# Performance work log

Hardware: AMD Instinct MI355X
Metric: run time of the kernel (lower is better)

## Reference

```python
import jax, jax.numpy as jnp
import numpy as np

B, SQ, SK, D, H = 2, 2048, 2048, 1024, 16
DK = D // H


def setup_inputs() -> dict:
    key = jax.random.key(0)
    ks = jax.random.split(key, 16)
    s = 1.0 / np.sqrt(D)
    inp = {
        "query": jax.random.normal(ks[0], (B, SQ, D), jnp.float32),
        "key": jax.random.normal(ks[1], (B, SK, D), jnp.float32),
        "value": jax.random.normal(ks[2], (B, SK, D), jnp.float32),
        "R": jax.random.normal(ks[3], (B, SK, D), jnp.float32),
        "Wq": jax.random.normal(ks[4], (D, D), jnp.float32) * s,
        "bq": jnp.zeros((D,), jnp.float32),
        "Wv": jax.random.normal(ks[5], (D, D), jnp.float32) * s,
        "bv": jnp.zeros((D,), jnp.float32),
        "Wr": jax.random.normal(ks[6], (D, D), jnp.float32) * s,
        "br": jnp.zeros((D,), jnp.float32),
        "W_h": jax.random.normal(ks[7], (H, DK, DK), jnp.float32) * (1.0 / np.sqrt(DK)),
        "Wo": jax.random.normal(ks[8], (D, D), jnp.float32) * s,
        "bo": jnp.zeros((D,), jnp.float32),
    }
    return inp


def _forward(query, key, value, R, Wq, bq, Wv, bv, Wr, br, W_h, Wo, bo):
    scale = 1.0 / np.sqrt(DK)
    # projections (torch Linear: x @ W.T + b)
    Q = (query @ Wq.T + bq).reshape(B, SQ, H, DK).transpose(0, 2, 1, 3)   # (B,H,SQ,DK)
    V = (value @ Wv.T + bv).reshape(B, SK, H, DK).transpose(0, 2, 1, 3)   # (B,H,SK,DK)
    Rp = (R @ Wr.T + br).reshape(B, SK, H, DK).transpose(0, 2, 1, 3)      # (B,H,SK,DK)
    # torch einsum 'hnk,bhn->bhn' sums W_h over its last axis -> elementwise gate
    w_rowsum = W_h.sum(axis=-1)  # (H, DK)

    def step(h, r_t):
        h_new = jnp.tanh(h * w_rowsum + r_t)  # (B,H,DK)
        return h_new, h_new

    h0 = jnp.zeros((B, H, DK), Rp.dtype)
    Rt = Rp.transpose(2, 0, 1, 3)  # (SK,B,H,DK)
    _, Hs = jax.lax.scan(step, h0, Rt)
    Hst = Hs.transpose(1, 2, 0, 3)  # (B,H,SK,DK)

    scores = jnp.einsum('bhqd,bhkd->bhqk', Q, Hst) * scale
    attn = jax.nn.softmax(scores, axis=-1)
    out = jnp.einsum('bhqk,bhkd->bhqd', attn, V)
    out = out.transpose(0, 2, 1, 3).reshape(B, SQ, D)
    return out @ Wo.T + bo


def reference(query, key, value, R, Wq, bq, Wv, bv, Wr, br, W_h, Wo, bo):
    return _forward(query, key, value, R, Wq, bq, Wv, bv, Wr, br, W_h, Wo, bo)
```

## Files before the change

### kernel.cpp

```cpp
#include <hip/hip_runtime.h>
#include <stdint.h>

typedef unsigned short u16;
typedef __attribute__((ext_vector_type(8))) _Float16 h8;
typedef __attribute__((ext_vector_type(2))) __fp16 hp2;
typedef __attribute__((ext_vector_type(4))) float f4;

#define B_ 2
#define SQ_ 2048
#define SK_ 2048
#define D_ 1024
#define H_ 16
#define DK_ 64

__device__ __forceinline__ u16 f2h(float f) {
  union { _Float16 h; u16 u; } v; v.h = (_Float16)f; return v.u;
}
__device__ __forceinline__ float h2f(u16 b) {
  union { u16 u; _Float16 h; } v; v.u = b; return (float)v.h;
}
__device__ __forceinline__ unsigned pkrtz(float a, float b) {
  union { hp2 h; unsigned u; } v; v.h = __builtin_amdgcn_cvt_pkrtz(a, b); return v.u;
}
__device__ __forceinline__ float fexp2(float x) {
  float r;
  asm("v_exp_f32 %0, %1" : "=v"(r) : "v"(x));
  return r;
}

typedef const void __attribute__((address_space(1)))* gas1;
typedef void __attribute__((address_space(3)))* las3;
__device__ __forceinline__ void gld16(const void* g, void* l) {
  __builtin_amdgcn_global_load_lds((gas1)g, (las3)l, 16, 0, 0);
}

__device__ __forceinline__ void cast8(const float* __restrict__ src,
                                      u16* __restrict__ dst, int i) {
  float4 a = *(const float4*)(src + i);
  float4 b = *(const float4*)(src + i + 4);
  alignas(16) u16 t[8] = {f2h(a.x), f2h(a.y), f2h(a.z), f2h(a.w),
                          f2h(b.x), f2h(b.y), f2h(b.z), f2h(b.w)};
  *(int4*)(dst + i) = *(int4*)t;
}

__global__ void rma_cast_rwr(const float* __restrict__ xr, const float* __restrict__ wr,
                             u16* __restrict__ orr, u16* __restrict__ owr) {
  const int b = blockIdx.x;
  const float* src; u16* dst; int bi;
  if (b < 2048) { src = xr; dst = orr; bi = b; }
  else          { src = wr; dst = owr; bi = b - 2048; }
  cast8(src, dst, (bi * 256 + threadIdx.x) * 8);
}

__device__ __forceinline__ void gemm_mainloop(
    const u16* __restrict__ A, const u16* __restrict__ Bw, int K,
    u16* As, u16* Bs, int m0, int n0, f4 (&acc)[4][4]) {
  const int tid = threadIdx.x;
  const int w = tid >> 6, lane = tid & 63;
  const int quad = lane >> 4, ln = lane & 15;
  const int wm = (w >> 1) * 64, wn = (w & 1) * 64;
  const int c0 = tid, c1 = tid + 256;
  const u16* a0 = A + (size_t)(m0 + (c0 >> 2)) * K + (c0 & 3) * 8;
  const u16* a1 = A + (size_t)(m0 + (c1 >> 2)) * K + (c1 & 3) * 8;
  const u16* b0 = Bw + (size_t)(n0 + (c0 >> 2)) * K + (c0 & 3) * 8;
  const u16* b1 = Bw + (size_t)(n0 + (c1 >> 2)) * K + (c1 & 3) * 8;
  u16* As0 = As + (0 + w * 64) * 8;
  u16* As1 = As + (256 + w * 64) * 8;
  u16* Bs0 = Bs + (0 + w * 64) * 8;
  u16* Bs1 = Bs + (256 + w * 64) * 8;
  for (int kt = 0; kt < K; kt += 32) {
    gld16(a0 + kt, As0);
    gld16(a1 + kt, As1);
    gld16(b0 + kt, Bs0);
    gld16(b1 + kt, Bs1);
    __syncthreads();
    h8 af[4], bf[4];
#pragma unroll
    for (int i = 0; i < 4; i++)
      af[i] = *(const h8*)&As[(wm + i * 16 + ln) * 32 + quad * 8];
#pragma unroll
    for (int i = 0; i < 4; i++)
      bf[i] = *(const h8*)&Bs[(wn + i * 16 + ln) * 32 + quad * 8];
#pragma unroll
    for (int i = 0; i < 4; i++)
#pragma unroll
      for (int j = 0; j < 4; j++)
        acc[i][j] = __builtin_amdgcn_mfma_f32_16x16x32_f16(af[i], bf[j], acc[i][j], 0, 0, 0);
    __syncthreads();
  }
}

__device__ __forceinline__ void gemm_mainloop64(
    const u16* __restrict__ A, const u16* __restrict__ Bw, int K,
    u16* As, u16* Bs, int m0, int n0, f4 (&acc)[2][4]) {
  const int tid = threadIdx.x;
  const int w = tid >> 6, lane = tid & 63;
  const int quad = lane >> 4, ln = lane & 15;
  const int wm = (w >> 1) * 32, wn = (w & 1) * 64;
  const u16* a0 = A + (size_t)(m0 + (tid >> 2)) * K + (tid & 3) * 8;
  const u16* b0 = Bw + (size_t)(n0 + (tid >> 2)) * K + (tid & 3) * 8;
  const u16* b1 = Bw + (size_t)(n0 + ((tid + 256) >> 2)) * K + (tid & 3) * 8;
  u16* As0 = As + (w * 64) * 8;
  u16* Bs0 = Bs + (w * 64) * 8;
  u16* Bs1 = Bs + (256 + w * 64) * 8;
  for (int kt = 0; kt < K; kt += 32) {
    gld16(a0 + kt, As0);
    gld16(b0 + kt, Bs0);
    gld16(b1 + kt, Bs1);
    __syncthreads();
    h8 af[2], bf[4];
#pragma unroll
    for (int i = 0; i < 2; i++)
      af[i] = *(const h8*)&As[(wm + i * 16 + ln) * 32 + quad * 8];
#pragma unroll
    for (int j = 0; j < 4; j++)
      bf[j] = *(const h8*)&Bs[(wn + j * 16 + ln) * 32 + quad * 8];
#pragma unroll
    for (int i = 0; i < 2; i++)
#pragma unroll
      for (int j = 0; j < 4; j++)
        acc[i][j] = __builtin_amdgcn_mfma_f32_16x16x32_f16(af[i], bf[j], acc[i][j], 0, 0, 0);
    __syncthreads();
  }
}

__global__ __launch_bounds__(256, 2)
void rma_projr_cast(const u16* __restrict__ Xr, const u16* __restrict__ Wrb,
                    const float* __restrict__ br, float* __restrict__ Rp,
                    const float* __restrict__ xq, const float* __restrict__ xv,
                    const float* __restrict__ wq, const float* __restrict__ wv,
                    const float* __restrict__ wo, u16* __restrict__ oxq,
                    u16* __restrict__ oxv, u16* __restrict__ owq,
                    u16* __restrict__ owv, u16* __restrict__ owo) {
  __shared__ u16 As[128 * 32];
  __shared__ u16 Bs[128 * 32];
  const int b = blockIdx.x;
  if (b >= 256) {
    const int c = b - 256;
    const float* src; u16* dst; int bi;
    if (c < 2048)       { src = xq; dst = oxq; bi = c; }
    else if (c < 4096)  { src = xv; dst = oxv; bi = c - 2048; }
    else if (c < 4608)  { src = wq; dst = owq; bi = c - 4096; }
    else if (c < 5120)  { src = wv; dst = owv; bi = c - 4608; }
    else                { src = wo; dst = owo; bi = c - 5120; }
    cast8(src, dst, (bi * 256 + threadIdx.x) * 8);
    return;
  }
  const int m0 = (b & 31) * 128, n0 = (b >> 5) * 128;
  f4 acc[4][4] = {};
  gemm_mainloop(Xr, Wrb, D_, As, Bs, m0, n0, acc);
  const int tid = threadIdx.x;
  const int w = tid >> 6, lane = tid & 63;
  const int quad = lane >> 4, ln = lane & 15;
  const int wm = (w >> 1) * 64, wn = (w & 1) * 64;
#pragma unroll
  for (int i = 0; i < 4; i++)
#pragma unroll
    for (int j = 0; j < 4; j++) {
      const int colg = n0 + wn + j * 16 + ln;
      const float bb = br[colg];
      const int h = colg >> 6, d = colg & 63;
      const int row4 = m0 + wm + i * 16 + quad * 4;
      const int bb_i = row4 >> 11, s = row4 & 2047;
#pragma unroll
      for (int r = 0; r < 4; r++) {
        const size_t idx = ((size_t)(bb_i * H_ + h) * SK_ + (s + r)) * DK_ + d;
        Rp[idx] = acc[i][j][r] + bb;
      }
    }
}

#define RB_ 32
__global__ __launch_bounds__(256, 1)
void rma_recur_projqv(const float* __restrict__ Rp, const float* __restrict__ Wh,
                      u16* __restrict__ Hst, const u16* __restrict__ Xq,
                      const u16* __restrict__ Xv, const u16* __restrict__ Wqb,
                      const u16* __restrict__ Wvb, const float* __restrict__ bq,
                      const float* __restrict__ bv, u16* __restrict__ Qb,
                      u16* __restrict__ Vt) {
  __shared__ u16 As[128 * 32];
  __shared__ u16 Bs[128 * 32];
  const int blk = blockIdx.x;
  if (blk < 8) {
    __builtin_amdgcn_s_setprio(2);
    const int ch = blk * 256 + threadIdx.x;
    const int bh = ch >> 6, d = ch & 63, h = bh & 15;
    const float* wr = Wh + (h * 64 + d) * 64;
    float ws = 0.f;
#pragma unroll
    for (int k = 0; k < 64; k += 4) {
      float4 wv4 = *(const float4*)(wr + k);
      ws += (wv4.x + wv4.y) + (wv4.z + wv4.w);
    }
    const float C2 = 2.885390081777927f;
    const float wsC2 = ws * C2;
    const float Kw = 2.0f * wsC2;
    const size_t base = (size_t)bh * (SK_ * DK_) + d;
    const float* r = Rp + base;
    u16* o = Hst + base;
    float cur[RB_], nxt[RB_];
#pragma unroll
    for (int j = 0; j < RB_; j++) cur[j] = r[(size_t)j * DK_];
    float e = fexp2(cur[0] * C2);
    for (int t0 = 0; t0 < SK_; t0 += RB_) {
      const int tn = (t0 + RB_ < SK_) ? (t0 + RB_) : t0;
#pragma unroll
      for (int j = 0; j < RB_; j++) nxt[j] = r[(size_t)(tn + j) * DK_];
#pragma unroll
      for (int j = 0; j < RB_; j++) {
        const float a = e + 1.0f;
        const float bb = __builtin_amdgcn_rcpf(a);
        const float hs = __builtin_fmaf(-2.0f, bb, 1.0f);
        o[(size_t)(t0 + j) * DK_] = f2h(hs);
        const float rn = (j + 1 < RB_) ? cur[j + 1] : nxt[0];
        const float K = __builtin_fmaf(C2, rn, wsC2);
        const float x = __builtin_fmaf(-Kw, bb, K);
        e = fexp2(x);
      }
#pragma unroll
      for (int j = 0; j < RB_; j++) cur[j] = nxt[j];
    }
    return;
  }
  const int pb = blk - 8;
  const int z = pb >> 8;
  const int t = pb & 255;
  const int m0 = (t & 31) * 128, n0 = (t >> 5) * 128;
  const u16* A = z == 0 ? Xq : Xv;
  const u16* Bw = z == 0 ? Wqb : Wvb;
  const float* bias = z == 0 ? bq : bv;
  f4 acc[4][4] = {};
  gemm_mainloop(A, Bw, D_, As, Bs, m0, n0, acc);
  const int tid = threadIdx.x;
  const int w = tid >> 6, lane = tid & 63;
  const int quad = lane >> 4, ln = lane & 15;
  const int wm = (w >> 1) * 64, wn = (w & 1) * 64;
#pragma unroll
  for (int i = 0; i < 4; i++)
#pragma unroll
    for (int j = 0; j < 4; j++) {
      const int colg = n0 + wn + j * 16 + ln;
      const float bb = bias[colg];
      const int h = colg >> 6, d = colg & 63;
      const int row4 = m0 + wm + i * 16 + quad * 4;
      const int b = row4 >> 11, s = row4 & 2047;
      if (z == 1) {
        uint2 pk;
        pk.x = pkrtz(acc[i][j][0] + bb, acc[i][j][1] + bb);
        pk.y = pkrtz(acc[i][j][2] + bb, acc[i][j][3] + bb);
        *(uint2*)&Vt[((size_t)((b * H_ + h) * DK_ + d)) * SK_ + s] = pk;
      } else {
#pragma unroll
        for (int r = 0; r < 4; r++) {
          const float v = acc[i][j][r] + bb;
          const size_t idx = ((size_t)(b * H_ + h) * SK_ + (s + r)) * DK_ + d;
          Qb[idx] = f2h(v);
        }
      }
    }
}

__global__ __launch_bounds__(256, 2)
void rma_final_gemm(const u16* __restrict__ Og, const u16* __restrict__ Wo,
                    const float* __restrict__ bo, float* __restrict__ out) {
  __shared__ u16 As[64 * 32];
  __shared__ u16 Bs[128 * 32];
  const int m0 = blockIdx.x * 64, n0 = blockIdx.y * 128;
  f4 acc[2][4] = {};
  gemm_mainloop64(Og, Wo, D_, As, Bs, m0, n0, acc);
  const int tid = threadIdx.x;
  const int w = tid >> 6, lane = tid & 63;
  const int quad = lane >> 4, ln = lane & 15;
  const int wm = (w >> 1) * 32, wn = (w & 1) * 64;
#pragma unroll
  for (int i = 0; i < 2; i++)
#pragma unroll
    for (int j = 0; j < 4; j++) {
      const int colg = n0 + wn + j * 16 + ln;
      const float bb = bo[colg];
#pragma unroll
      for (int r = 0; r < 4; r++) {
        const int rowg = m0 + wm + i * 16 + quad * 4 + r;
        out[(size_t)rowg * D_ + colg] = acc[i][j][r] + bb;
      }
    }
}

#define FXM_ 12.0f
__global__ __launch_bounds__(256, 2)
void rma_flash(const u16* __restrict__ Qb, const u16* __restrict__ Hst,
               const u16* __restrict__ Vt, u16* __restrict__ Og) {
  __shared__ u16 Kt[64 * 72];
  __shared__ u16 Vts[64 * 72];
  __shared__ u16 Ps[4][32 * 72];
  const int tid = threadIdx.x;
  const int w = tid >> 6, lane = tid & 63;
  const int quad = lane >> 4, ln = lane & 15;
  const int bh = blockIdx.y;
  const int q0 = blockIdx.x * 128 + w * 32;
  const float scale2 = 0.18033688011112042f;
  const u16* Qg = Qb + (size_t)bh * SQ_ * DK_;
  const u16* Kg = Hst + (size_t)bh * SK_ * DK_;
  const u16* Vg = Vt + (size_t)bh * DK_ * SK_;
  u16* Pw = Ps[w];
  h8 qf[2][2];
#pragma unroll
  for (int qt = 0; qt < 2; qt++)
#pragma unroll
    for (int c = 0; c < 2; c++)
      qf[qt][c] = *(const h8*)&Qg[(size_t)(q0 + qt * 16 + ln) * DK_ + c * 32 + quad * 8];
  f4 o[4][2] = {};
  float l[2] = {0.f, 0.f};

  const int c0 = tid, c1 = tid + 256;
  const int r0 = c0 >> 3, o0 = (c0 & 7) * 8;
  const int r1 = c1 >> 3, o1 = (c1 & 7) * 8;
  const u16* kg0 = Kg + (size_t)r0 * DK_ + o0;
  const u16* kg1 = Kg + (size_t)r1 * DK_ + o1;
  const u16* vg0 = Vg + (size_t)r0 * SK_ + o0;
  const u16* vg1 = Vg + (size_t)r1 * SK_ + o1;
  u16* kl0 = &Kt[r0 * 72 + o0];
  u16* kl1 = &Kt[r1 * 72 + o1];
  u16* vl0 = &Vts[r0 * 72 + o0];
  u16* vl1 = &Vts[r1 * 72 + o1];

  int4 ks0 = *(const int4*)(kg0);
  int4 ks1 = *(const int4*)(kg1);
  int4 vs0 = *(const int4*)(vg0);
  int4 vs1 = *(const int4*)(vg1);

  for (int kt = 0; kt < SK_; kt += 64) {
    __syncthreads();
    *(int4*)kl0 = ks0;
    *(int4*)kl1 = ks1;
    *(int4*)vl0 = vs0;
    *(int4*)vl1 = vs1;
    __syncthreads();
    h8 kf[4][2], vf[4][2];
#pragma unroll
    for (int m = 0; m < 4; m++) {
      kf[m][0] = *(const h8*)&Kt[(m * 16 + ln) * 72 + quad * 8];
      kf[m][1] = *(const h8*)&Kt[(m * 16 + ln) * 72 + 32 + quad * 8];
    }
#pragma unroll
    for (int dt = 0; dt < 4; dt++) {
      vf[dt][0] = *(const h8*)&Vts[(dt * 16 + ln) * 72 + quad * 8];
      vf[dt][1] = *(const h8*)&Vts[(dt * 16 + ln) * 72 + 32 + quad * 8];
    }
    const int ktn = (kt + 64 < SK_) ? kt + 64 : 0;
    ks0 = *(const int4*)(kg0 + (size_t)ktn * DK_);
    ks1 = *(const int4*)(kg1 + (size_t)ktn * DK_);
    vs0 = *(const int4*)(vg0 + ktn);
    vs1 = *(const int4*)(vg1 + ktn);
    f4 st[4][2];
#pragma unroll
    for (int m = 0; m < 4; m++)
#pragma unroll
      for (int qt = 0; qt < 2; qt++) {
        f4 t = {0.f, 0.f, 0.f, 0.f};
        t = __builtin_amdgcn_mfma_f32_16x16x32_f16(kf[m][0], qf[qt][0], t, 0, 0, 0);
        t = __builtin_amdgcn_mfma_f32_16x16x32_f16(kf[m][1], qf[qt][1], t, 0, 0, 0);
        st[m][qt] = t;
      }
#pragma unroll
    for (int qt = 0; qt < 2; qt++)
#pragma unroll
      for (int m = 0; m < 4; m++) {
        const float p0 = fexp2(__builtin_fmaf(st[m][qt][0], scale2, -FXM_));
        const float p1 = fexp2(__builtin_fmaf(st[m][qt][1], scale2, -FXM_));
        const float p2 = fexp2(__builtin_fmaf(st[m][qt][2], scale2, -FXM_));
        const float p3 = fexp2(__builtin_fmaf(st[m][qt][3], scale2, -FXM_));
        l[qt] += (p0 + p1) + (p2 + p3);
        uint2 pk;
        pk.x = pkrtz(p0, p1);
        pk.y = pkrtz(p2, p3);
        *(uint2*)&Pw[(qt * 16 + ln) * 72 + m * 16 + quad * 4] = pk;
      }
    asm volatile("" ::: "memory");
#pragma unroll
    for (int c = 0; c < 2; c++) {
      h8 pb0 = *(const h8*)&Pw[(0 + ln) * 72 + c * 32 + quad * 8];
      h8 pb1 = *(const h8*)&Pw[(16 + ln) * 72 + c * 32 + quad * 8];
#pragma unroll
      for (int dt = 0; dt < 4; dt++) {
        o[dt][0] = __builtin_amdgcn_mfma_f32_16x16x32_f16(vf[dt][c], pb0, o[dt][0], 0, 0, 0);
        o[dt][1] = __builtin_amdgcn_mfma_f32_16x16x32_f16(vf[dt][c], pb1, o[dt][1], 0, 0, 0);
      }
    }
  }
  const int b = bh >> 4, h = bh & 15;
#pragma unroll
  for (int qt = 0; qt < 2; qt++) {
    float lq = l[qt];
    lq += __shfl_xor(lq, 16);
    lq += __shfl_xor(lq, 32);
    const float linv = __builtin_amdgcn_rcpf(lq);
    const int q = q0 + qt * 16 + ln;
#pragma unroll
    for (int dt = 0; dt < 4; dt++) {
      uint2 pk;
      pk.x = pkrtz(o[dt][qt][0] * linv, o[dt][qt][1] * linv);
      pk.y = pkrtz(o[dt][qt][2] * linv, o[dt][qt][3] * linv);
      *(uint2*)&Og[((size_t)b * SQ_ + q) * D_ + h * DK_ + dt * 16 + quad * 4] = pk;
    }
  }
}

extern "C" void kernel_launch(void* const* d_in, const int* in_sizes, int n_in,
                              void* d_out, int out_size, void* d_ws, size_t ws_size,
                              hipStream_t stream) {
  const float* query = (const float*)d_in[0];
  const float* value = (const float*)d_in[2];
  const float* R = (const float*)d_in[3];
  const float* Wq = (const float*)d_in[4];
  const float* bq = (const float*)d_in[5];
  const float* Wv = (const float*)d_in[6];
  const float* bv = (const float*)d_in[7];
  const float* Wr = (const float*)d_in[8];
  const float* br = (const float*)d_in[9];
  const float* W_h = (const float*)d_in[10];
  const float* Wo = (const float*)d_in[11];
  const float* bo = (const float*)d_in[12];
  float* out = (float*)d_out;

  char* ws = (char*)d_ws;
  const size_t MB = 1 << 20;
  u16* Xq = (u16*)(ws + 0 * MB);
  u16* Xv = (u16*)(ws + 8 * MB);
  u16* Xr = (u16*)(ws + 16 * MB);
  u16* Wqb = (u16*)(ws + 24 * MB);
  u16* Wvb = (u16*)(ws + 26 * MB);
  u16* Wrb = (u16*)(ws + 28 * MB);
  u16* Wob = (u16*)(ws + 30 * MB);
  u16* Qb = (u16*)(ws + 32 * MB);
  u16* Vt = (u16*)(ws + 40 * MB);
  float* Rp = (float*)(ws + 48 * MB);
  u16* Hs = (u16*)(ws + 64 * MB);
  u16* Og = (u16*)(ws + 72 * MB);

  rma_cast_rwr<<<dim3(2560), 256, 0, stream>>>(R, Wr, Xr, Wrb);
  rma_projr_cast<<<dim3(5888), 256, 0, stream>>>(Xr, Wrb, br, Rp,
                                                 query, value, Wq, Wv, Wo,
                                                 Xq, Xv, Wqb, Wvb, Wob);
  rma_recur_projqv<<<dim3(520), 256, 72 * 1024, stream>>>(Rp, W_h, Hs, Xq, Xv,
                                                          Wqb, Wvb, bq, bv, Qb, Vt);
  rma_flash<<<dim3(16, 32), 256, 0, stream>>>(Qb, Hs, Vt, Og);
  rma_final_gemm<<<dim3(64, 8), 256, 0, stream>>>(Og, Wob, bo, out);
}
```

Baseline: 287.9 us.

## Fuse projection, recurrence and flash stages into a persistent ticket-scheduled megakernel

Three kernels (R projection plus casts, recurrence plus Q/V projection, flash attention) become one persistent kernel. Blocks pull tasks from an atomic ticket counter and wait on device-scope progress counters, so the recurrence can start on R chunks as soon as they are projected and flash tiles can consume hidden states while the recurrence is still running. GEMM tiles grow to 256x128 with 512 threads, and the flash loop drops its register prefetch in favour of gated loads. The cost is spin-wait overhead, a serialised recurrence held on 4 blocks, and a deadlock risk if the resident-block assumptions do not hold.

```diff
diff --git a/kernel.cpp b/kernel.cpp
--- a/kernel.cpp
+++ b/kernel.cpp
@@ -13,11 +13,18 @@
 #define H_ 16
 #define DK_ 64
 
+#define C_TICKET 0
+#define C_CAST   1
+#define C_PROJ   2
+#define C_RDONE  3
+#define C_PROG   19
+#define T_CAST0  128
+#define T_PQV0   480
+#define T_FLASH0 736
+#define T_END    992
+
 __device__ __forceinline__ u16 f2h(float f) {
   union { _Float16 h; u16 u; } v; v.h = (_Float16)f; return v.u;
-}
-__device__ __forceinline__ float h2f(u16 b) {
-  union { u16 u; _Float16 h; } v; v.u = b; return (float)v.h;
 }
 __device__ __forceinline__ unsigned pkrtz(float a, float b) {
   union { hp2 h; unsigned u; } v; v.h = __builtin_amdgcn_cvt_pkrtz(a, b); return v.u;
@@ -32,6 +39,18 @@
 typedef void __attribute__((address_space(3)))* las3;
 __device__ __forceinline__ void gld16(const void* g, void* l) {
   __builtin_amdgcn_global_load_lds((gas1)g, (las3)l, 16, 0, 0);
+}
+
+__device__ __forceinline__ void spin_ge(int* p, int v) {
+  if (__hip_atomic_load(p, __ATOMIC_RELAXED, __HIP_MEMORY_SCOPE_AGENT) >= v) return;
+  int n = 0;
+  for (;;) {
+    __builtin_amdgcn_s_sleep(8);
+    int x = ((++n & 63) == 0)
+                ? __hip_atomic_load(p, __ATOMIC_ACQUIRE, __HIP_MEMORY_SCOPE_AGENT)
+                : __hip_atomic_load(p, __ATOMIC_RELAXED, __HIP_MEMORY_SCOPE_AGENT);
+    if (x >= v) return;
+  }
 }
 
 __device__ __forceinline__ void cast8(const float* __restrict__ src,
@@ -43,44 +62,44 @@
   *(int4*)(dst + i) = *(int4*)t;
 }
 
-__global__ void rma_cast_rwr(const float* __restrict__ xr, const float* __restrict__ wr,
-                             u16* __restrict__ orr, u16* __restrict__ owr) {
+__global__ void rma_cast_init(const float* __restrict__ xr, const float* __restrict__ wr,
+                              u16* __restrict__ orr, u16* __restrict__ owr,
+                              int* __restrict__ ctrl) {
   const int b = blockIdx.x;
+  if (b == 0 && threadIdx.x < 64) ctrl[threadIdx.x] = 0;
   const float* src; u16* dst; int bi;
   if (b < 2048) { src = xr; dst = orr; bi = b; }
   else          { src = wr; dst = owr; bi = b - 2048; }
   cast8(src, dst, (bi * 256 + threadIdx.x) * 8);
 }
 
-__device__ __forceinline__ void gemm_mainloop(
-    const u16* __restrict__ A, const u16* __restrict__ Bw, int K,
-    u16* As, u16* Bs, int m0, int n0, f4 (&acc)[4][4]) {
-  const int tid = threadIdx.x;
-  const int w = tid >> 6, lane = tid & 63;
+__device__ __forceinline__ void gemm_super(const u16* __restrict__ A,
+                                           const u16* __restrict__ Bw,
+                                           u16* As, u16* Bs, int m0, int n0,
+                                           f4 (&acc)[4][4]) {
+  const int tid = threadIdx.x;
+  const int w8 = tid >> 6, lane = tid & 63;
   const int quad = lane >> 4, ln = lane & 15;
-  const int wm = (w >> 1) * 64, wn = (w & 1) * 64;
-  const int c0 = tid, c1 = tid + 256;
-  const u16* a0 = A + (size_t)(m0 + (c0 >> 2)) * K + (c0 & 3) * 8;
-  const u16* a1 = A + (size_t)(m0 + (c1 >> 2)) * K + (c1 & 3) * 8;
-  const u16* b0 = Bw + (size_t)(n0 + (c0 >> 2)) * K + (c0 & 3) * 8;
-  const u16* b1 = Bw + (size_t)(n0 + (c1 >> 2)) * K + (c1 & 3) * 8;
-  u16* As0 = As + (0 + w * 64) * 8;
-  u16* As1 = As + (256 + w * 64) * 8;
-  u16* Bs0 = Bs + (0 + w * 64) * 8;
-  u16* Bs1 = Bs + (256 + w * 64) * 8;
-  for (int kt = 0; kt < K; kt += 32) {
+  const int wm = (w8 >> 1) * 64, wn = (w8 & 1) * 64;
+  const int c0 = tid, c1 = tid + 512;
+  const u16* a0 = A + (size_t)(m0 + (c0 >> 2)) * D_ + (c0 & 3) * 8;
+  const u16* a1 = A + (size_t)(m0 + (c1 >> 2)) * D_ + (c1 & 3) * 8;
+  const u16* b0 = Bw + (size_t)(n0 + (c0 >> 2)) * D_ + (c0 & 3) * 8;
+  u16* As0 = As + (size_t)(w8 * 64) * 8;
+  u16* As1 = As + (size_t)(512 + w8 * 64) * 8;
+  u16* Bs0 = Bs + (size_t)(w8 * 64) * 8;
+  for (int kt = 0; kt < D_; kt += 32) {
     gld16(a0 + kt, As0);
     gld16(a1 + kt, As1);
     gld16(b0 + kt, Bs0);
-    gld16(b1 + kt, Bs1);
     __syncthreads();
     h8 af[4], bf[4];
 #pragma unroll
     for (int i = 0; i < 4; i++)
       af[i] = *(const h8*)&As[(wm + i * 16 + ln) * 32 + quad * 8];
 #pragma unroll
-    for (int i = 0; i < 4; i++)
-      bf[i] = *(const h8*)&Bs[(wn + i * 16 + ln) * 32 + quad * 8];
+    for (int j = 0; j < 4; j++)
+      bf[j] = *(const h8*)&Bs[(wn + j * 16 + ln) * 32 + quad * 8];
 #pragma unroll
     for (int i = 0; i < 4; i++)
 #pragma unroll
@@ -124,185 +143,72 @@
   }
 }
 
-__global__ __launch_bounds__(256, 2)
-void rma_projr_cast(const u16* __restrict__ Xr, const u16* __restrict__ Wrb,
-                    const float* __restrict__ br, float* __restrict__ Rp,
-                    const float* __restrict__ xq, const float* __restrict__ xv,
-                    const float* __restrict__ wq, const float* __restrict__ wv,
-                    const float* __restrict__ wo, u16* __restrict__ oxq,
-                    u16* __restrict__ oxv, u16* __restrict__ owq,
-                    u16* __restrict__ owv, u16* __restrict__ owo) {
-  __shared__ u16 As[128 * 32];
-  __shared__ u16 Bs[128 * 32];
-  const int b = blockIdx.x;
-  if (b >= 256) {
-    const int c = b - 256;
-    const float* src; u16* dst; int bi;
-    if (c < 2048)       { src = xq; dst = oxq; bi = c; }
-    else if (c < 4096)  { src = xv; dst = oxv; bi = c - 2048; }
-    else if (c < 4608)  { src = wq; dst = owq; bi = c - 4096; }
-    else if (c < 5120)  { src = wv; dst = owv; bi = c - 4608; }
-    else                { src = wo; dst = owo; bi = c - 5120; }
-    cast8(src, dst, (bi * 256 + threadIdx.x) * 8);
-    return;
-  }
-  const int m0 = (b & 31) * 128, n0 = (b >> 5) * 128;
-  f4 acc[4][4] = {};
-  gemm_mainloop(Xr, Wrb, D_, As, Bs, m0, n0, acc);
-  const int tid = threadIdx.x;
-  const int w = tid >> 6, lane = tid & 63;
+#define RB_ 32
+__device__ void recur_run(const float* __restrict__ Rp, const float* __restrict__ Wh,
+                          u16* __restrict__ Hst, int* ctrl) {
+  const int tid = threadIdx.x;
+  const int ch = blockIdx.x * 512 + tid;
+  const int bh = ch >> 6, d = ch & 63, h = bh & 15, b = bh >> 4;
+  const float* wr = Wh + (h * 64 + d) * 64;
+  float ws = 0.f;
+#pragma unroll
+  for (int k = 0; k < 64; k += 4) {
+    float4 wv4 = *(const float4*)(wr + k);
+    ws += (wv4.x + wv4.y) + (wv4.z + wv4.w);
+  }
+  const float C2 = 2.885390081777927f;
+  const float wsC2 = ws * C2;
+  const float Kw = 2.0f * wsC2;
+  const size_t base = (size_t)bh * (SK_ * DK_) + d;
+  const float* r = Rp + base;
+  u16* o = Hst + base;
+  int* rd = ctrl + C_RDONE + b * 8;
+  int* pg = ctrl + C_PROG + bh;
+  spin_ge(&rd[0], 8);
+  float cur[RB_], nxt[RB_];
+#pragma unroll
+  for (int j = 0; j < RB_; j++) cur[j] = r[(size_t)j * DK_];
+  float e = fexp2(cur[0] * C2);
+  for (int t0 = 0; t0 < SK_; t0 += RB_) {
+    const int t1 = t0 + RB_;
+    if (t1 < SK_ && ((t1 & 255) == 0)) spin_ge(&rd[t1 >> 8], 8);
+    const int tn = (t1 < SK_) ? t1 : t0;
+#pragma unroll
+    for (int j = 0; j < RB_; j++) nxt[j] = r[(size_t)(tn + j) * DK_];
+#pragma unroll
+    for (int j = 0; j < RB_; j++) {
+      const float a = e + 1.0f;
+      const float bb = __builtin_amdgcn_rcpf(a);
+      const float hs = __builtin_fmaf(-2.0f, bb, 1.0f);
+      o[(size_t)(t0 + j) * DK_] = f2h(hs);
+      const float rn = (j + 1 < RB_) ? cur[j + 1] : nxt[0];
+      const float K = __builtin_fmaf(C2, rn, wsC2);
+      const float x = __builtin_fmaf(-Kw, bb, K);
+      e = fexp2(x);
+    }
+    if (((t1 & 127) == 0) && (tid & 63) == 0)
+      __hip_atomic_store(pg, t1, __ATOMIC_RELEASE, __HIP_MEMORY_SCOPE_AGENT);
+#pragma unroll
+    for (int j = 0; j < RB_; j++) cur[j] = nxt[j];
+  }
+}
+
+#define FXM_ 12.0f
+__device__ void flash_task(int fidx, const u16* __restrict__ Qb,
+                           const u16* __restrict__ Hst, const u16* __restrict__ Vt,
+                           u16* __restrict__ Og, u16* smem, int* ctrl) {
+  const int tid = threadIdx.x;
+  const int w8 = tid >> 6, lane = tid & 63;
   const int quad = lane >> 4, ln = lane & 15;
-  const int wm = (w >> 1) * 64, wn = (w & 1) * 64;
-#pragma unroll
-  for (int i = 0; i < 4; i++)
-#pragma unroll
-    for (int j = 0; j < 4; j++) {
-      const int colg = n0 + wn + j * 16 + ln;
-      const float bb = br[colg];
-      const int h = colg >> 6, d = colg & 63;
-      const int row4 = m0 + wm + i * 16 + quad * 4;
-      const int bb_i = row4 >> 11, s = row4 & 2047;
-#pragma unroll
-      for (int r = 0; r < 4; r++) {
-        const size_t idx = ((size_t)(bb_i * H_ + h) * SK_ + (s + r)) * DK_ + d;
-        Rp[idx] = acc[i][j][r] + bb;
-      }
-    }
-}
-
-#define RB_ 32
-__global__ __launch_bounds__(256, 1)
-void rma_recur_projqv(const float* __restrict__ Rp, const float* __restrict__ Wh,
-                      u16* __restrict__ Hst, const u16* __restrict__ Xq,
-                      const u16* __restrict__ Xv, const u16* __restrict__ Wqb,
-                      const u16* __restrict__ Wvb, const float* __restrict__ bq,
-                      const float* __restrict__ bv, u16* __restrict__ Qb,
-                      u16* __restrict__ Vt) {
-  __shared__ u16 As[128 * 32];
-  __shared__ u16 Bs[128 * 32];
-  const int blk = blockIdx.x;
-  if (blk < 8) {
-    __builtin_amdgcn_s_setprio(2);
-    const int ch = blk * 256 + threadIdx.x;
-    const int bh = ch >> 6, d = ch & 63, h = bh & 15;
-    const float* wr = Wh + (h * 64 + d) * 64;
-    float ws = 0.f;
-#pragma unroll
-    for (int k = 0; k < 64; k += 4) {
-      float4 wv4 = *(const float4*)(wr + k);
-      ws += (wv4.x + wv4.y) + (wv4.z + wv4.w);
-    }
-    const float C2 = 2.885390081777927f;
-    const float wsC2 = ws * C2;
-    const float Kw = 2.0f * wsC2;
-    const size_t base = (size_t)bh * (SK_ * DK_) + d;
-    const float* r = Rp + base;
-    u16* o = Hst + base;
-    float cur[RB_], nxt[RB_];
-#pragma unroll
-    for (int j = 0; j < RB_; j++) cur[j] = r[(size_t)j * DK_];
-    float e = fexp2(cur[0] * C2);
-    for (int t0 = 0; t0 < SK_; t0 += RB_) {
-      const int tn = (t0 + RB_ < SK_) ? (t0 + RB_) : t0;
-#pragma unroll
-      for (int j = 0; j < RB_; j++) nxt[j] = r[(size_t)(tn + j) * DK_];
-#pragma unroll
-      for (int j = 0; j < RB_; j++) {
-        const float a = e + 1.0f;
-        const float bb = __builtin_amdgcn_rcpf(a);
-        const float hs = __builtin_fmaf(-2.0f, bb, 1.0f);
-        o[(size_t)(t0 + j) * DK_] = f2h(hs);
-        const float rn = (j + 1 < RB_) ? cur[j + 1] : nxt[0];
-        const float K = __builtin_fmaf(C2, rn, wsC2);
-        const float x = __builtin_fmaf(-Kw, bb, K);
-        e = fexp2(x);
-      }
-#pragma unroll
-      for (int j = 0; j < RB_; j++) cur[j] = nxt[j];
-    }
-    return;
-  }
-  const int pb = blk - 8;
-  const int z = pb >> 8;
-  const int t = pb & 255;
-  const int m0 = (t & 31) * 128, n0 = (t >> 5) * 128;
-  const u16* A = z == 0 ? Xq : Xv;
-  const u16* Bw = z == 0 ? Wqb : Wvb;
-  const float* bias = z == 0 ? bq : bv;
-  f4 acc[4][4] = {};
-  gemm_mainloop(A, Bw, D_, As, Bs, m0, n0, acc);
-  const int tid = threadIdx.x;
-  const int w = tid >> 6, lane = tid & 63;
-  const int quad = lane >> 4, ln = lane & 15;
-  const int wm = (w >> 1) * 64, wn = (w & 1) * 64;
-#pragma unroll
-  for (int i = 0; i < 4; i++)
-#pragma unroll
-    for (int j = 0; j < 4; j++) {
-      const int colg = n0 + wn + j * 16 + ln;
-      const float bb = bias[colg];
-      const int h = colg >> 6, d = colg & 63;
-      const int row4 = m0 + wm + i * 16 + quad * 4;
-      const int b = row4 >> 11, s = row4 & 2047;
-      if (z == 1) {
-        uint2 pk;
-        pk.x = pkrtz(acc[i][j][0] + bb, acc[i][j][1] + bb);
-        pk.y = pkrtz(acc[i][j][2] + bb, acc[i][j][3] + bb);
-        *(uint2*)&Vt[((size_t)((b * H_ + h) * DK_ + d)) * SK_ + s] = pk;
-      } else {
-#pragma unroll
-        for (int r = 0; r < 4; r++) {
-          const float v = acc[i][j][r] + bb;
-          const size_t idx = ((size_t)(b * H_ + h) * SK_ + (s + r)) * DK_ + d;
-          Qb[idx] = f2h(v);
-        }
-      }
-    }
-}
-
-__global__ __launch_bounds__(256, 2)
-void rma_final_gemm(const u16* __restrict__ Og, const u16* __restrict__ Wo,
-                    const float* __restrict__ bo, float* __restrict__ out) {
-  __shared__ u16 As[64 * 32];
-  __shared__ u16 Bs[128 * 32];
-  const int m0 = blockIdx.x * 64, n0 = blockIdx.y * 128;
-  f4 acc[2][4] = {};
-  gemm_mainloop64(Og, Wo, D_, As, Bs, m0, n0, acc);
-  const int tid = threadIdx.x;
-  const int w = tid >> 6, lane = tid & 63;
-  const int quad = lane >> 4, ln = lane & 15;
-  const int wm = (w >> 1) * 32, wn = (w & 1) * 64;
-#pragma unroll
-  for (int i = 0; i < 2; i++)
-#pragma unroll
-    for (int j = 0; j < 4; j++) {
-      const int colg = n0 + wn + j * 16 + ln;
-      const float bb = bo[colg];
-#pragma unroll
-      for (int r = 0; r < 4; r++) {
-        const int rowg = m0 + wm + i * 16 + quad * 4 + r;
-        out[(size_t)rowg * D_ + colg] = acc[i][j][r] + bb;
-      }
-    }
-}
-
-#define FXM_ 12.0f
-__global__ __launch_bounds__(256, 2)
-void rma_flash(const u16* __restrict__ Qb, const u16* __restrict__ Hst,
-               const u16* __restrict__ Vt, u16* __restrict__ Og) {
-  __shared__ u16 Kt[64 * 72];
-  __shared__ u16 Vts[64 * 72];
-  __shared__ u16 Ps[4][32 * 72];
-  const int tid = threadIdx.x;
-  const int w = tid >> 6, lane = tid & 63;
-  const int quad = lane >> 4, ln = lane & 15;
-  const int bh = blockIdx.y;
-  const int q0 = blockIdx.x * 128 + w * 32;
+  const int bh = fidx >> 3, qq = fidx & 7;
+  const int q0 = qq * 256 + w8 * 32;
+  u16* Kt = smem;
+  u16* Vts = smem + 64 * 72;
+  u16* Pw = smem + 2 * 64 * 72 + w8 * (32 * 72);
   const float scale2 = 0.18033688011112042f;
   const u16* Qg = Qb + (size_t)bh * SQ_ * DK_;
   const u16* Kg = Hst + (size_t)bh * SK_ * DK_;
   const u16* Vg = Vt + (size_t)bh * DK_ * SK_;
-  u16* Pw = Ps[w];
   h8 qf[2][2];
 #pragma unroll
   for (int qt = 0; qt < 2; qt++)
@@ -311,30 +217,19 @@
       qf[qt][c] = *(const h8*)&Qg[(size_t)(q0 + qt * 16 + ln) * DK_ + c * 32 + quad * 8];
   f4 o[4][2] = {};
   float l[2] = {0.f, 0.f};
-
-  const int c0 = tid, c1 = tid + 256;
-  const int r0 = c0 >> 3, o0 = (c0 & 7) * 8;
-  const int r1 = c1 >> 3, o1 = (c1 & 7) * 8;
+  const int r0 = tid >> 3, o0 = (tid & 7) * 8;
   const u16* kg0 = Kg + (size_t)r0 * DK_ + o0;
-  const u16* kg1 = Kg + (size_t)r1 * DK_ + o1;
   const u16* vg0 = Vg + (size_t)r0 * SK_ + o0;
-  const u16* vg1 = Vg + (size_t)r1 * SK_ + o1;
   u16* kl0 = &Kt[r0 * 72 + o0];
-  u16* kl1 = &Kt[r1 * 72 + o1];
   u16* vl0 = &Vts[r0 * 72 + o0];
-  u16* vl1 = &Vts[r1 * 72 + o1];
-
-  int4 ks0 = *(const int4*)(kg0);
-  int4 ks1 = *(const int4*)(kg1);
-  int4 vs0 = *(const int4*)(vg0);
-  int4 vs1 = *(const int4*)(vg1);
-
+  int* pg = ctrl + C_PROG + bh;
   for (int kt = 0; kt < SK_; kt += 64) {
-    __syncthreads();
-    *(int4*)kl0 = ks0;
-    *(int4*)kl1 = ks1;
-    *(int4*)vl0 = vs0;
-    *(int4*)vl1 = vs1;
+    if (tid == 0) spin_ge(pg, kt + 64);
+    __syncthreads();
+    int4 ks = *(const int4*)(kg0 + (size_t)kt * DK_);
+    int4 vs = *(const int4*)(vg0 + kt);
+    *(int4*)kl0 = ks;
+    *(int4*)vl0 = vs;
     __syncthreads();
     h8 kf[4][2], vf[4][2];
 #pragma unroll
@@ -347,11 +242,6 @@
       vf[dt][0] = *(const h8*)&Vts[(dt * 16 + ln) * 72 + quad * 8];
       vf[dt][1] = *(const h8*)&Vts[(dt * 16 + ln) * 72 + 32 + quad * 8];
     }
-    const int ktn = (kt + 64 < SK_) ? kt + 64 : 0;
-    ks0 = *(const int4*)(kg0 + (size_t)ktn * DK_);
-    ks1 = *(const int4*)(kg1 + (size_t)ktn * DK_);
-    vs0 = *(const int4*)(vg0 + ktn);
-    vs1 = *(const int4*)(vg1 + ktn);
     f4 st[4][2];
 #pragma unroll
     for (int m = 0; m < 4; m++)
@@ -404,6 +294,143 @@
       *(uint2*)&Og[((size_t)b * SQ_ + q) * D_ + h * DK_ + dt * 16 + quad * 4] = pk;
     }
   }
+}
+
+__global__ __launch_bounds__(512, 2)
+void rma_mega(const float* __restrict__ query, const float* __restrict__ value,
+              const float* __restrict__ Wq, const float* __restrict__ Wv,
+              const float* __restrict__ Wo, u16* __restrict__ Xq,
+              u16* __restrict__ Xv, u16* __restrict__ Wqb, u16* __restrict__ Wvb,
+              u16* __restrict__ Wob, const u16* __restrict__ Xr,
+              const u16* __restrict__ Wrb, const float* __restrict__ br,
+              float* __restrict__ Rp, const float* __restrict__ Wh,
+              u16* __restrict__ Hst, const float* __restrict__ bq,
+              const float* __restrict__ bv, u16* __restrict__ Qb,
+              u16* __restrict__ Vt, u16* __restrict__ Og, int* ctrl) {
+  __shared__ __align__(16) u16 smem[43008];
+  __shared__ int s_t;
+  const int tid = threadIdx.x;
+  if (blockIdx.x < 4) {
+    recur_run(Rp, Wh, Hst, ctrl);
+    return;
+  }
+  u16* As = smem;
+  u16* Bs = smem + 8192;
+  for (;;) {
+    __syncthreads();
+    if (tid == 0) s_t = atomicAdd(&ctrl[C_TICKET], 1);
+    __syncthreads();
+    const int t = s_t;
+    if (t >= T_END) return;
+    if (t < T_CAST0) {
+      const int m_s = t & 15, n0 = (t >> 4) << 7, m0 = m_s << 8;
+      f4 acc[4][4] = {};
+      gemm_super(Xr, Wrb, As, Bs, m0, n0, acc);
+      const int w8 = tid >> 6, lane = tid & 63;
+      const int quad = lane >> 4, ln = lane & 15;
+      const int wm = (w8 >> 1) * 64, wn = (w8 & 1) * 64;
+#pragma unroll
+      for (int i = 0; i < 4; i++)
+#pragma unroll
+        for (int j = 0; j < 4; j++) {
+          const int colg = n0 + wn + j * 16 + ln;
+          const float bb = br[colg];
+          const int h = colg >> 6, d = colg & 63;
+          const int row4 = m0 + wm + i * 16 + quad * 4;
+          const int b = row4 >> 11, s = row4 & 2047;
+#pragma unroll
+          for (int r = 0; r < 4; r++)
+            Rp[((size_t)(b * H_ + h) * SK_ + (s + r)) * DK_ + d] = acc[i][j][r] + bb;
+        }
+      __syncthreads();
+      if (tid == 0)
+        __hip_atomic_fetch_add(&ctrl[C_RDONE + m_s], 1, __ATOMIC_RELEASE,
+                               __HIP_MEMORY_SCOPE_AGENT);
+    } else if (t < T_PQV0) {
+      const int ci = t - T_CAST0;
+      const float* src; u16* dst; int off;
+      if (ci < 128)      { src = query; dst = Xq;  off = ci << 15; }
+      else if (ci < 256) { src = value; dst = Xv;  off = (ci - 128) << 15; }
+      else if (ci < 288) { src = Wq;    dst = Wqb; off = (ci - 256) << 15; }
+      else if (ci < 320) { src = Wv;    dst = Wvb; off = (ci - 288) << 15; }
+      else               { src = Wo;    dst = Wob; off = (ci - 320) << 15; }
+#pragma unroll
+      for (int it = 0; it < 8; it++) cast8(src, dst, off + it * 4096 + tid * 8);
+      __syncthreads();
+      if (tid == 0)
+        __hip_atomic_fetch_add(&ctrl[C_CAST], 1, __ATOMIC_RELEASE,
+                               __HIP_MEMORY_SCOPE_AGENT);
+    } else if (t < T_FLASH0) {
+      const int idx = t - T_PQV0;
+      const int z = idx >> 7, sdec = idx & 127;
+      const int m_s = sdec & 15, n0 = (sdec >> 4) << 7, m0 = m_s << 8;
+      if (tid == 0) spin_ge(&ctrl[C_CAST], 352);
+      __syncthreads();
+      const u16* A = z == 0 ? Xq : Xv;
+      const u16* Bw = z == 0 ? Wqb : Wvb;
+      const float* bias = z == 0 ? bq : bv;
+      f4 acc[4][4] = {};
+      gemm_super(A, Bw, As, Bs, m0, n0, acc);
+      const int w8 = tid >> 6, lane = tid & 63;
+      const int quad = lane >> 4, ln = lane & 15;
+      const int wm = (w8 >> 1) * 64, wn = (w8 & 1) * 64;
+#pragma unroll
+      for (int i = 0; i < 4; i++)
+#pragma unroll
+        for (int j = 0; j < 4; j++) {
+          const int colg = n0 + wn + j * 16 + ln;
+          const float bb = bias[colg];
+          const int h = colg >> 6, d = colg & 63;
+          const int row4 = m0 + wm + i * 16 + quad * 4;
+          const int b = row4 >> 11, s = row4 & 2047;
+          if (z == 1) {
+            uint2 pk;
+            pk.x = pkrtz(acc[i][j][0] + bb, acc[i][j][1] + bb);
+            pk.y = pkrtz(acc[i][j][2] + bb, acc[i][j][3] + bb);
+            *(uint2*)&Vt[((size_t)((b * H_ + h) * DK_ + d)) * SK_ + s] = pk;
+          } else {
+#pragma unroll
+            for (int r = 0; r < 4; r++)
+              Qb[((size_t)(b * H_ + h) * SK_ + (s + r)) * DK_ + d] =
+                  f2h(acc[i][j][r] + bb);
+          }
+        }
+      __syncthreads();
+      if (tid == 0)
+        __hip_atomic_fetch_add(&ctrl[C_PROJ], 1, __ATOMIC_RELEASE,
+                               __HIP_MEMORY_SCOPE_AGENT);
+    } else {
+      if (tid == 0) spin_ge(&ctrl[C_PROJ], 256);
+      __syncthreads();
+      flash_task(t - T_FLASH0, Qb, Hst, Vt, Og, smem, ctrl);
+    }
+  }
+}
+
+__global__ __launch_bounds__(256, 2)
+void rma_final_gemm(const u16* __restrict__ Og, const u16* __restrict__ Wo,
+                    const float* __restrict__ bo, float* __restrict__ out) {
+  __shared__ u16 As[64 * 32];
+  __shared__ u16 Bs[128 * 32];
+  const int m0 = blockIdx.x * 64, n0 = blockIdx.y * 128;
+  f4 acc[2][4] = {};
+  gemm_mainloop64(Og, Wo, D_, As, Bs, m0, n0, acc);
+  const int tid = threadIdx.x;
+  const int w = tid >> 6, lane = tid & 63;
+  const int quad = lane >> 4, ln = lane & 15;
+  const int wm = (w >> 1) * 32, wn = (w & 1) * 64;
+#pragma unroll
+  for (int i = 0; i < 2; i++)
+#pragma unroll
+    for (int j = 0; j < 4; j++) {
+      const int colg = n0 + wn + j * 16 + ln;
+      const float bb = bo[colg];
+#pragma unroll
+      for (int r = 0; r < 4; r++) {
+        const int rowg = m0 + wm + i * 16 + quad * 4 + r;
+        out[(size_t)rowg * D_ + colg] = acc[i][j][r] + bb;
+      }
+    }
 }
 
 extern "C" void kernel_launch(void* const* d_in, const int* in_sizes, int n_in,
@@ -437,13 +464,11 @@
   float* Rp = (float*)(ws + 48 * MB);
   u16* Hs = (u16*)(ws + 64 * MB);
   u16* Og = (u16*)(ws + 72 * MB);
-
-  rma_cast_rwr<<<dim3(2560), 256, 0, stream>>>(R, Wr, Xr, Wrb);
-  rma_projr_cast<<<dim3(5888), 256, 0, stream>>>(Xr, Wrb, br, Rp,
-                                                 query, value, Wq, Wv, Wo,
-                                                 Xq, Xv, Wqb, Wvb, Wob);
-  rma_recur_projqv<<<dim3(520), 256, 72 * 1024, stream>>>(Rp, W_h, Hs, Xq, Xv,
-                                                          Wqb, Wvb, bq, bv, Qb, Vt);
-  rma_flash<<<dim3(16, 32), 256, 0, stream>>>(Qb, Hs, Vt, Og);
+  int* ctrl = (int*)(ws + 80 * MB);
+
+  rma_cast_init<<<dim3(2560), 256, 0, stream>>>(R, Wr, Xr, Wrb, ctrl);
+  rma_mega<<<dim3(256), 512, 0, stream>>>(query, value, Wq, Wv, Wo, Xq, Xv, Wqb,
+                                          Wvb, Wob, Xr, Wrb, br, Rp, W_h, Hs, bq,
+                                          bv, Qb, Vt, Og, ctrl);
   rma_final_gemm<<<dim3(64, 8), 256, 0, stream>>>(Og, Wob, bo, out);
 }
```

After: 388.1 us. +34.8%, slower.
